# Optimization experiments

Measured on AMD Instinct MI355X. Metric: run time of the kernel, lower is better.

## Reference

```python
import jax, jax.numpy as jnp
import numpy as np

LOG2PI = float(np.log(2.0 * np.pi))


def setup_inputs() -> dict:
    key = jax.random.key(0)
    k1, k2, k3 = jax.random.split(key, 3)
    batch, dim_z, n_samples = 1024, 32, 32
    mean = jax.random.normal(k1, (batch, dim_z), dtype=jnp.float32)
    logvar = jax.random.normal(k2, (batch, dim_z), dtype=jnp.float32)
    eps = jax.random.normal(k3, (batch, n_samples, dim_z), dtype=jnp.float32)
    return {"mean": mean, "logvar": logvar, "eps": eps,
            "n_samples": n_samples, "agg_size": 256}


def reference(mean, logvar, eps, n_samples, agg_size):
    batch, dim_z = mean.shape
    if batch % agg_size != 0:
        agg_size = batch
    nc = batch // agg_size  # num_chunks
    # GaussianReParameterize: z ~ N(mean, exp(logvar)), shape [B, n_samples, dim_z]
    std = jnp.exp(0.5 * logvar)
    z = mean[:, None, :] + eps * std[:, None, :]
    # z2: [nc, agg_size*n_samples, dim_z]
    z2 = z.reshape(nc, agg_size * n_samples, dim_z)
    # component params broadcast against all samples in the chunk
    mu = mean.reshape(nc, agg_size, 1, dim_z)
    lv = logvar.reshape(nc, agg_size, 1, dim_z)
    # per-dimension Gaussian log-PDF of each sample under each component:
    # [nc, agg_size, agg_size*n_samples, dim_z]
    log_q_ijk = -0.5 * ((z2[:, None, :, :] - mu) ** 2 * jnp.exp(-lv) + lv + LOG2PI)
    # mixture density per dimension: mean over components, then log, then mean over samples
    logq = jnp.log(jnp.exp(log_q_ijk).mean(axis=1)).mean(axis=1)  # [nc, dim_z]
    # log standard-normal density per dimension, averaged over samples
    logp = (-0.5 * (z2 ** 2 + LOG2PI)).mean(axis=1)  # [nc, dim_z]
    okl = (logq - logp).mean(axis=0)  # [dim_z]
    return okl.sum(axis=-1)
```

## Files before the change

kernel.cpp:

```cpp
#include <hip/hip_runtime.h>
#include <math.h>

#define B    1024
#define D    32
#define AGG  256
#define NC   4
#define M    8192
#define NEV  1024

#define TN     512
#define ZMIN   (-32.0f)
#define INVH   8.0f
#define HH     0.125f
#define ZCLAMP 31.8f

#define WS_TABLE 8192
#define WS_NEED  (8192 + 128 * TN * 8)

#define LOG2E 1.4426950408889634f
#define LN2   0.6931471805599453f

__global__ __launch_bounds__(1024) void ktable2(const float* __restrict__ mean,
                                                const float* __restrict__ logvar,
                                                float2* __restrict__ table)
{
    const int ck   = blockIdx.x;
    const int t    = threadIdx.x;
    const int lane = t & 63;
    const int wv   = t >> 6;

    __shared__ float4 ps[AGG];
    if (t < AGG) {
        const int c   = ck >> 5;
        const int k   = ck & (D - 1);
        const int row = (c << 8) + t;
        const float mu = mean[row * D + k];
        const float lv = logvar[row * D + k];
        const float ev = __builtin_amdgcn_exp2f(-lv * LOG2E);
        const float A  = -0.5f * LOG2E * ev;
        ps[t] = make_float4(A, LOG2E * mu * ev,
                            -0.5f * LOG2E * fmaf(mu * mu, ev, lv),
                            __builtin_amdgcn_exp2f(A * (2.f * HH * HH)));
    }
    __syncthreads();

    const int g0   = lane << 3;
    const float z0 = fmaf((float)g0, HH, ZMIN);
    const float tz = z0 + z0 + HH;
    float a0 = 0.f, a1 = 0.f, a2 = 0.f, a3 = 0.f;
    float a4 = 0.f, a5 = 0.f, a6 = 0.f, a7 = 0.f;
    float d0 = 0.f, d1 = 0.f, d2 = 0.f, d3 = 0.f;
    float d4 = 0.f, d5 = 0.f, d6 = 0.f, d7 = 0.f;
#pragma unroll
    for (int i = 0; i < 16; ++i) {
        const float4 p = ps[(wv << 4) + i];
        const float ap = fmaf(p.x, z0, p.y);
        float w = __builtin_amdgcn_exp2f(fmaf(ap, z0, p.z));
        float dd = HH * fmaf(p.x, tz, p.y);
        dd = fminf(dd, 126.f);
        float r = __builtin_amdgcn_exp2f(dd);
        const float qd = p.x * (2.f * HH);
        float q = fmaf(p.x, z0, ap);
        a0 += w; d0 = fmaf(w, q, d0); q += qd;
        w *= r; a1 += w; d1 = fmaf(w, q, d1); q += qd; r *= p.w;
        w *= r; a2 += w; d2 = fmaf(w, q, d2); q += qd; r *= p.w;
        w *= r; a3 += w; d3 = fmaf(w, q, d3); q += qd; r *= p.w;
        w *= r; a4 += w; d4 = fmaf(w, q, d4); q += qd; r *= p.w;
        w *= r; a5 += w; d5 = fmaf(w, q, d5); q += qd; r *= p.w;
        w *= r; a6 += w; d6 = fmaf(w, q, d6); q += qd; r *= p.w;
        w *= r; a7 += w; d7 = fmaf(w, q, d7);
    }

    __shared__ float2 part[16][TN];
    {
        float2* pb = &part[wv][g0];
        pb[0] = make_float2(a0, d0); pb[1] = make_float2(a1, d1);
        pb[2] = make_float2(a2, d2); pb[3] = make_float2(a3, d3);
        pb[4] = make_float2(a4, d4); pb[5] = make_float2(a5, d5);
        pb[6] = make_float2(a6, d6); pb[7] = make_float2(a7, d7);
    }
    __syncthreads();
    if (t < TN) {
        float s = 0.f, d = 0.f;
#pragma unroll
        for (int w = 0; w < 16; ++w) {
            const float2 pw = part[w][t];
            s += pw.x; d += pw.y;
        }
        const float sg = fmaxf(s, 1e-30f);
        table[(ck << 9) | t] =
            make_float2(__builtin_amdgcn_logf(sg),
                        d * __builtin_amdgcn_rcpf(sg) * HH);
    }
}

__global__ __launch_bounds__(256) void keval2(const float* __restrict__ eps,
                                              const float* __restrict__ mean,
                                              const float* __restrict__ logvar,
                                              const float2* __restrict__ table,
                                              float* __restrict__ partial)
{
    const int t    = threadIdx.x;
    const int gidx = (blockIdx.x * 256 + t) << 2;
    const int c    = gidx >> 18;
    const int r18  = gidx & 262143;
    const int j    = r18 >> 5;
    const int k0   = r18 & 31;
    const int row  = (c << 8) + (j >> 5);
    const int ckb  = (c << 5) + k0;

    const float4 e4 = *(const float4*)(eps + gidx);
    const float4 m4 = *(const float4*)(mean + row * D + k0);
    const float4 l4 = *(const float4*)(logvar + row * D + k0);
    const float e[4]  = {e4.x, e4.y, e4.z, e4.w};
    const float mu[4] = {m4.x, m4.y, m4.z, m4.w};
    const float lv[4] = {l4.x, l4.y, l4.z, l4.w};

    float r = 0.f;
#pragma unroll
    for (int kk = 0; kk < 4; ++kk) {
        const float sd = __builtin_amdgcn_exp2f(0.5f * LOG2E * lv[kk]);
        const float z  = fmaf(e[kk], sd, mu[kk]);
        const float zc = fminf(fmaxf(z, -ZCLAMP), ZCLAMP);
        const float x  = fmaf(zc, INVH, 256.0f);
        const float fg = floorf(x);
        const float f  = x - fg;
        const int  ig  = (int)fg;
        const float2* __restrict__ tg = table + ((ckb + kk) << 9);
        const float2 n0 = tg[ig];
        const float2 n1 = tg[ig + 1];
        const float dl  = n1.x - n0.x;
        const float c2  = 3.f * dl - 2.f * n0.y - n1.y;
        const float c3  = n0.y + n1.y - 2.f * dl;
        const float L   = fmaf(f, fmaf(f, fmaf(f, c3, c2), n0.y), n0.x);
        r += fmaf(LN2, L, 0.5f * z * z);
    }

    for (int off = 32; off > 0; off >>= 1) r += __shfl_down(r, off, 64);
    __shared__ float wsum[4];
    if ((t & 63) == 0) wsum[t >> 6] = r;
    __syncthreads();
    if (t == 0) partial[blockIdx.x] = (wsum[0] + wsum[1]) + (wsum[2] + wsum[3]);
}

__global__ __launch_bounds__(256) void kfinal(const float* __restrict__ partial,
                                              float* __restrict__ out)
{
    const int t = threadIdx.x;
    double s = 0.0;
#pragma unroll
    for (int i = 0; i < NEV / 256; ++i) s += (double)partial[i * 256 + t];
    __shared__ double sd[256];
    sd[t] = s;
    __syncthreads();
    for (int off = 128; off > 0; off >>= 1) {
        if (t < off) sd[t] += sd[t + off];
        __syncthreads();
    }
    if (t == 0)
        out[0] = (float)(sd[0] * (1.0 / (double)(NC * M))
                         - (double)D * 5.545177444479562);
}

__global__ __launch_bounds__(256) void kfb(const float* __restrict__ eps,
                                           const float* __restrict__ mean,
                                           const float* __restrict__ logvar,
                                           float* __restrict__ partial)
{
    const int bid = blockIdx.x;
    const int ck  = bid >> 3;
    const int q   = bid & 7;
    const int c   = ck >> 5;
    const int k   = ck & (D - 1);
    const int j0  = q << 10;
    const int t   = threadIdx.x;

    __shared__ float4 prm[AGG];
    {
        const int row  = (c << 8) + t;
        const float mu = mean[row * D + k];
        const float lv = logvar[row * D + k];
        const float ev = __builtin_amdgcn_exp2f(-lv * LOG2E);
        prm[t] = make_float4(-0.5f * LOG2E * ev, LOG2E * mu * ev,
                             -0.5f * LOG2E * fmaf(mu * mu, ev, lv),
                             __builtin_amdgcn_exp2f(0.5f * LOG2E * lv));
    }
    __syncthreads();

    float zv[4], acc[4];
#pragma unroll
    for (int u = 0; u < 4; ++u) {
        const int j    = j0 + t + (u << 8);
        const float4 p = prm[j >> 5];
        const float mu = -0.5f * p.y * __builtin_amdgcn_rcpf(p.x);
        zv[u]  = fmaf(eps[(size_t)((c << 13) + j) * D + k], p.w, mu);
        acc[u] = 0.f;
    }
#pragma unroll 4
    for (int i = 0; i < AGG; ++i) {
        const float4 p = prm[i];
#pragma unroll
        for (int u = 0; u < 4; ++u)
            acc[u] += __builtin_amdgcn_exp2f(fmaf(fmaf(p.x, zv[u], p.y), zv[u], p.z));
    }
    float r = 0.f;
#pragma unroll
    for (int u = 0; u < 4; ++u)
        r += LN2 * __builtin_amdgcn_logf(acc[u]) + 0.5f * zv[u] * zv[u];

    for (int off = 32; off > 0; off >>= 1) r += __shfl_down(r, off, 64);
    __shared__ float wsum[4];
    if ((t & 63) == 0) wsum[t >> 6] = r;
    __syncthreads();
    if (t == 0) partial[bid] = (wsum[0] + wsum[1]) + (wsum[2] + wsum[3]);
}

extern "C" void kernel_launch(void* const* d_in, const int* in_sizes, int n_in,
                              void* d_out, int out_size, void* d_ws, size_t ws_size,
                              hipStream_t stream)
{
    const float* mean   = (const float*)d_in[0];
    const float* logvar = (const float*)d_in[1];
    const float* eps    = (const float*)d_in[2];
    float* out = (float*)d_out;

    float*  partial = (float*)d_ws;
    float2* table   = (float2*)((char*)d_ws + WS_TABLE);

    if (ws_size >= (size_t)WS_NEED) {
        ktable2<<<128, 1024, 0, stream>>>(mean, logvar, table);
        keval2<<<NEV, 256, 0, stream>>>(eps, mean, logvar, table, partial);
    } else {
        kfb<<<NEV, 256, 0, stream>>>(eps, mean, logvar, partial);
    }
    kfinal<<<1, 256, 0, stream>>>(partial, out);
}
```

Measured before the change: 17.35 us.

## Transpose eps per dimension so eval blocks stage one table in LDS

Adds a transpose kernel that rewrites eps into a [chunk, dim, sample] layout in workspace. The eval kernel is restructured so each block handles one (chunk, dim) pair, copies that pair's 512-entry log-density table into shared memory and does its lookups there instead of gathering from global memory. The cost is an extra kernel launch and an extra full read and write of eps (4 MB) through global memory, plus a larger workspace requirement.

Result: slower. 20.93 us (+20.6%).

```diff
diff --git a/kernel.cpp b/kernel.cpp
--- a/kernel.cpp
+++ b/kernel.cpp
@@ -15,7 +15,8 @@
 #define ZCLAMP 31.8f
 
 #define WS_TABLE 8192
-#define WS_NEED  (8192 + 128 * TN * 8)
+#define WS_EPST  532480
+#define WS_NEED  4726784
 
 #define LOG2E 1.4426950408889634f
 #define LN2   0.6931471805599453f
@@ -94,41 +95,71 @@
     }
 }
 
-__global__ __launch_bounds__(256) void keval2(const float* __restrict__ eps,
-                                              const float* __restrict__ mean,
-                                              const float* __restrict__ logvar,
-                                              const float2* __restrict__ table,
-                                              float* __restrict__ partial)
-{
-    const int t    = threadIdx.x;
-    const int gidx = (blockIdx.x * 256 + t) << 2;
-    const int c    = gidx >> 18;
-    const int r18  = gidx & 262143;
-    const int j    = r18 >> 5;
-    const int k0   = r18 & 31;
-    const int row  = (c << 8) + (j >> 5);
-    const int ckb  = (c << 5) + k0;
-
-    const float4 e4 = *(const float4*)(eps + gidx);
-    const float4 m4 = *(const float4*)(mean + row * D + k0);
-    const float4 l4 = *(const float4*)(logvar + row * D + k0);
-    const float e[4]  = {e4.x, e4.y, e4.z, e4.w};
-    const float mu[4] = {m4.x, m4.y, m4.z, m4.w};
-    const float lv[4] = {l4.x, l4.y, l4.z, l4.w};
-
+__global__ __launch_bounds__(256) void ktrans(const float* __restrict__ eps,
+                                              float* __restrict__ epsT)
+{
+    const int bid = blockIdx.x;
+    const int c   = bid >> 8;
+    const int j0t = (bid & 255) << 5;
+    const int t   = threadIdx.x;
+    const int x   = t & 31;
+    const int y0  = t >> 5;
+    __shared__ float tile[32][33];
+#pragma unroll
+    for (int p = 0; p < 4; ++p) {
+        const int r = (p << 3) + y0;
+        tile[r][x] = eps[((size_t)c * M + j0t + r) * D + x];
+    }
+    __syncthreads();
+#pragma unroll
+    for (int p = 0; p < 4; ++p) {
+        const int kk = (p << 3) + y0;
+        epsT[(((size_t)c * D + kk) << 13) + j0t + x] = tile[x][kk];
+    }
+}
+
+__global__ __launch_bounds__(256) void keval(const float* __restrict__ epsT,
+                                             const float* __restrict__ mean,
+                                             const float* __restrict__ logvar,
+                                             const float2* __restrict__ table,
+                                             float* __restrict__ partial)
+{
+    const int bid = blockIdx.x;
+    const int ck  = bid >> 3;
+    const int q   = bid & 7;
+    const int j0  = q << 10;
+    const int t   = threadIdx.x;
+
+    const float4 e4 = *(const float4*)(epsT + ((size_t)ck << 13) + j0 + (t << 2));
+    const float e[4] = {e4.x, e4.y, e4.z, e4.w};
+
+    __shared__ float2 rowp[32];
+    if (t < 32) {
+        const int c   = ck >> 5;
+        const int k   = ck & (D - 1);
+        const int row = (c << 8) + (q << 5) + t;
+        rowp[t] = make_float2(mean[row * D + k],
+                              __builtin_amdgcn_exp2f(0.5f * LOG2E * logvar[row * D + k]));
+    }
+
+    __shared__ float2 tab[TN];
+    const float2* __restrict__ gt = table + (ck << 9);
+    tab[t]       = gt[t];
+    tab[t + 256] = gt[t + 256];
+    __syncthreads();
+
+    const float2 ms = rowp[t >> 3];
     float r = 0.f;
 #pragma unroll
-    for (int kk = 0; kk < 4; ++kk) {
-        const float sd = __builtin_amdgcn_exp2f(0.5f * LOG2E * lv[kk]);
-        const float z  = fmaf(e[kk], sd, mu[kk]);
+    for (int u = 0; u < 4; ++u) {
+        const float z  = fmaf(e[u], ms.y, ms.x);
         const float zc = fminf(fmaxf(z, -ZCLAMP), ZCLAMP);
         const float x  = fmaf(zc, INVH, 256.0f);
         const float fg = floorf(x);
         const float f  = x - fg;
         const int  ig  = (int)fg;
-        const float2* __restrict__ tg = table + ((ckb + kk) << 9);
-        const float2 n0 = tg[ig];
-        const float2 n1 = tg[ig + 1];
+        const float2 n0 = tab[ig];
+        const float2 n1 = tab[ig + 1];
         const float dl  = n1.x - n0.x;
         const float c2  = 3.f * dl - 2.f * n0.y - n1.y;
         const float c3  = n0.y + n1.y - 2.f * dl;
@@ -140,7 +171,7 @@
     __shared__ float wsum[4];
     if ((t & 63) == 0) wsum[t >> 6] = r;
     __syncthreads();
-    if (t == 0) partial[blockIdx.x] = (wsum[0] + wsum[1]) + (wsum[2] + wsum[3]);
+    if (t == 0) partial[bid] = (wsum[0] + wsum[1]) + (wsum[2] + wsum[3]);
 }
 
 __global__ __launch_bounds__(256) void kfinal(const float* __restrict__ partial,
@@ -226,10 +257,12 @@
 
     float*  partial = (float*)d_ws;
     float2* table   = (float2*)((char*)d_ws + WS_TABLE);
+    float*  epsT    = (float*)((char*)d_ws + WS_EPST);
 
     if (ws_size >= (size_t)WS_NEED) {
         ktable2<<<128, 1024, 0, stream>>>(mean, logvar, table);
-        keval2<<<NEV, 256, 0, stream>>>(eps, mean, logvar, table, partial);
+        ktrans<<<NC * 256, 256, 0, stream>>>(eps, epsT);
+        keval<<<NEV, 256, 0, stream>>>(epsT, mean, logvar, table, partial);
     } else {
         kfb<<<NEV, 256, 0, stream>>>(eps, mean, logvar, partial);
     }
```

## Fuse final reduction into eval kernel via last-block atomic counter

Applied to the files above, without the earlier changes.

Drops the separate final-reduction kernel launch. The eval kernel now uses an atomic counter so the last block to finish sums the per-block partials and writes the output. The counter is reset at the start of the table kernel. The eval grid also shrinks from 1024 to 256 blocks, each handling four float4 groups per thread, so there are fewer partials to reduce. This saves one launch and its dependency gap, at the cost of less parallelism in the eval kernel and a serialized tail in the last block.

After: 21.55 us. +24.2%, slower.

```diff
diff --git a/kernel.cpp b/kernel.cpp
--- a/kernel.cpp
+++ b/kernel.cpp
@@ -6,7 +6,7 @@
 #define AGG  256
 #define NC   4
 #define M    8192
-#define NEV  1024
+#define NEV2 256
 
 #define TN     512
 #define ZMIN   (-32.0f)
@@ -22,12 +22,14 @@
 
 __global__ __launch_bounds__(1024) void ktable2(const float* __restrict__ mean,
                                                 const float* __restrict__ logvar,
-                                                float2* __restrict__ table)
+                                                float2* __restrict__ table,
+                                                unsigned* __restrict__ counter)
 {
     const int ck   = blockIdx.x;
     const int t    = threadIdx.x;
     const int lane = t & 63;
     const int wv   = t >> 6;
+    if (ck == 0 && t == 0) counter[0] = 0u;
 
     __shared__ float4 ps[AGG];
     if (t < AGG) {
@@ -98,68 +100,79 @@
                                               const float* __restrict__ mean,
                                               const float* __restrict__ logvar,
                                               const float2* __restrict__ table,
-                                              float* __restrict__ partial)
-{
-    const int t    = threadIdx.x;
-    const int gidx = (blockIdx.x * 256 + t) << 2;
-    const int c    = gidx >> 18;
-    const int r18  = gidx & 262143;
-    const int j    = r18 >> 5;
-    const int k0   = r18 & 31;
-    const int row  = (c << 8) + (j >> 5);
-    const int ckb  = (c << 5) + k0;
-
-    const float4 e4 = *(const float4*)(eps + gidx);
-    const float4 m4 = *(const float4*)(mean + row * D + k0);
-    const float4 l4 = *(const float4*)(logvar + row * D + k0);
-    const float e[4]  = {e4.x, e4.y, e4.z, e4.w};
-    const float mu[4] = {m4.x, m4.y, m4.z, m4.w};
-    const float lv[4] = {l4.x, l4.y, l4.z, l4.w};
+                                              float* __restrict__ partial,
+                                              unsigned* __restrict__ counter,
+                                              float* __restrict__ out)
+{
+    const int t   = threadIdx.x;
+    const int bid = blockIdx.x;
 
     float r = 0.f;
 #pragma unroll
-    for (int kk = 0; kk < 4; ++kk) {
-        const float sd = __builtin_amdgcn_exp2f(0.5f * LOG2E * lv[kk]);
-        const float z  = fmaf(e[kk], sd, mu[kk]);
-        const float zc = fminf(fmaxf(z, -ZCLAMP), ZCLAMP);
-        const float x  = fmaf(zc, INVH, 256.0f);
-        const float fg = floorf(x);
-        const float f  = x - fg;
-        const int  ig  = (int)fg;
-        const float2* __restrict__ tg = table + ((ckb + kk) << 9);
-        const float2 n0 = tg[ig];
-        const float2 n1 = tg[ig + 1];
-        const float dl  = n1.x - n0.x;
-        const float c2  = 3.f * dl - 2.f * n0.y - n1.y;
-        const float c3  = n0.y + n1.y - 2.f * dl;
-        const float L   = fmaf(f, fmaf(f, fmaf(f, c3, c2), n0.y), n0.x);
-        r += fmaf(LN2, L, 0.5f * z * z);
+    for (int u = 0; u < 4; ++u) {
+        const int gidx = (bid << 12) + (u << 10) + (t << 2);
+        const int c    = gidx >> 18;
+        const int r18  = gidx & 262143;
+        const int j    = r18 >> 5;
+        const int k0   = r18 & 31;
+        const int row  = (c << 8) + (j >> 5);
+        const int ckb  = (c << 5) + k0;
+
+        const float4 e4 = *(const float4*)(eps + gidx);
+        const float4 m4 = *(const float4*)(mean + row * D + k0);
+        const float4 l4 = *(const float4*)(logvar + row * D + k0);
+        const float e[4]  = {e4.x, e4.y, e4.z, e4.w};
+        const float mu[4] = {m4.x, m4.y, m4.z, m4.w};
+        const float lv[4] = {l4.x, l4.y, l4.z, l4.w};
+#pragma unroll
+        for (int kk = 0; kk < 4; ++kk) {
+            const float sd = __builtin_amdgcn_exp2f(0.5f * LOG2E * lv[kk]);
+            const float z  = fmaf(e[kk], sd, mu[kk]);
+            const float zc = fminf(fmaxf(z, -ZCLAMP), ZCLAMP);
+            const float x  = fmaf(zc, INVH, 256.0f);
+            const float fg = floorf(x);
+            const float f  = x - fg;
+            const int  ig  = (int)fg;
+            const float2* __restrict__ tg = table + ((ckb + kk) << 9);
+            const float2 n0 = tg[ig];
+            const float2 n1 = tg[ig + 1];
+            const float dl  = n1.x - n0.x;
+            const float c2  = 3.f * dl - 2.f * n0.y - n1.y;
+            const float c3  = n0.y + n1.y - 2.f * dl;
+            const float L   = fmaf(f, fmaf(f, fmaf(f, c3, c2), n0.y), n0.x);
+            r += fmaf(LN2, L, 0.5f * z * z);
+        }
     }
 
     for (int off = 32; off > 0; off >>= 1) r += __shfl_down(r, off, 64);
     __shared__ float wsum[4];
     if ((t & 63) == 0) wsum[t >> 6] = r;
     __syncthreads();
-    if (t == 0) partial[blockIdx.x] = (wsum[0] + wsum[1]) + (wsum[2] + wsum[3]);
-}
-
-__global__ __launch_bounds__(256) void kfinal(const float* __restrict__ partial,
-                                              float* __restrict__ out)
-{
-    const int t = threadIdx.x;
-    double s = 0.0;
-#pragma unroll
-    for (int i = 0; i < NEV / 256; ++i) s += (double)partial[i * 256 + t];
-    __shared__ double sd[256];
-    sd[t] = s;
-    __syncthreads();
-    for (int off = 128; off > 0; off >>= 1) {
-        if (t < off) sd[t] += sd[t + off];
+
+    __shared__ int isLast;
+    if (t == 0) {
+        const float v = (wsum[0] + wsum[1]) + (wsum[2] + wsum[3]);
+        __hip_atomic_store(&partial[bid], v, __ATOMIC_RELAXED,
+                           __HIP_MEMORY_SCOPE_AGENT);
+        const unsigned old = __hip_atomic_fetch_add(counter, 1u, __ATOMIC_ACQ_REL,
+                                                    __HIP_MEMORY_SCOPE_AGENT);
+        isLast = (old == (unsigned)(NEV2 - 1));
+    }
+    __syncthreads();
+    if (isLast) {
+        const float p = __hip_atomic_load(&partial[t], __ATOMIC_RELAXED,
+                                          __HIP_MEMORY_SCOPE_AGENT);
+        __shared__ double sd2[256];
+        sd2[t] = (double)p;
         __syncthreads();
-    }
-    if (t == 0)
-        out[0] = (float)(sd[0] * (1.0 / (double)(NC * M))
-                         - (double)D * 5.545177444479562);
+        for (int off = 128; off > 0; off >>= 1) {
+            if (t < off) sd2[t] += sd2[t + off];
+            __syncthreads();
+        }
+        if (t == 0)
+            out[0] = (float)(sd2[0] * (1.0 / (double)(NC * M))
+                             - (double)D * 5.545177444479562);
+    }
 }
 
 __global__ __launch_bounds__(256) void kfb(const float* __restrict__ eps,
@@ -215,6 +228,25 @@
     if (t == 0) partial[bid] = (wsum[0] + wsum[1]) + (wsum[2] + wsum[3]);
 }
 
+__global__ __launch_bounds__(256) void kfinal_fb(const float* __restrict__ partial,
+                                                 float* __restrict__ out)
+{
+    const int t = threadIdx.x;
+    double s = 0.0;
+#pragma unroll
+    for (int i = 0; i < 1024 / 256; ++i) s += (double)partial[i * 256 + t];
+    __shared__ double sd[256];
+    sd[t] = s;
+    __syncthreads();
+    for (int off = 128; off > 0; off >>= 1) {
+        if (t < off) sd[t] += sd[t + off];
+        __syncthreads();
+    }
+    if (t == 0)
+        out[0] = (float)(sd[0] * (1.0 / (double)(NC * M))
+                         - (double)D * 5.545177444479562);
+}
+
 extern "C" void kernel_launch(void* const* d_in, const int* in_sizes, int n_in,
                               void* d_out, int out_size, void* d_ws, size_t ws_size,
                               hipStream_t stream)
@@ -224,14 +256,16 @@
     const float* eps    = (const float*)d_in[2];
     float* out = (float*)d_out;
 
-    float*  partial = (float*)d_ws;
-    float2* table   = (float2*)((char*)d_ws + WS_TABLE);
+    unsigned* counter = (unsigned*)d_ws;
+    float*    partial = (float*)((char*)d_ws + 256);
+    float2*   table   = (float2*)((char*)d_ws + WS_TABLE);
 
     if (ws_size >= (size_t)WS_NEED) {
-        ktable2<<<128, 1024, 0, stream>>>(mean, logvar, table);
-        keval2<<<NEV, 256, 0, stream>>>(eps, mean, logvar, table, partial);
+        ktable2<<<128, 1024, 0, stream>>>(mean, logvar, table, counter);
+        keval2<<<NEV2, 256, 0, stream>>>(eps, mean, logvar, table,
+                                         partial, counter, out);
     } else {
-        kfb<<<NEV, 256, 0, stream>>>(eps, mean, logvar, partial);
-    }
-    kfinal<<<1, 256, 0, stream>>>(partial, out);
-}
+        kfb<<<1024, 256, 0, stream>>>(eps, mean, logvar, partial);
+        kfinal_fb<<<1, 256, 0, stream>>>(partial, out);
+    }
+}
```
